# Performance work log

Hardware: AMD Instinct MI355X
Metric: run time of the kernel (lower is better)

## Reference

```python
import jax, jax.numpy as jnp
import numpy as np

N_NODES = 50000
N_EDGES = 1000000


def _gat_layer(x, edge_index, edge_prob, W, Wt, a_src, a_trg, a_tp, b, Wskip, concat):
    """One GATLayerImp3 forward (eval mode, dropout=identity).
    x: [N,Fin], edge_index: [2,E] (row0=src,row1=trg), edge_prob: [E,1].
    a_*: [1,H,F]. Returns [N,H*F] if concat else [N,F]."""
    N = x.shape[0]
    H, F = a_src.shape[1], a_src.shape[2]
    src, trg = edge_index[0], edge_index[1]

    proj = (x @ W).reshape(N, H, F)                      # [N,H,F]
    tp_proj = (edge_prob @ Wt).reshape(-1, H, F)         # [E,H,F]

    s_src = jnp.sum(proj * a_src, axis=-1)               # [N,H]
    s_trg = jnp.sum(proj * a_trg, axis=-1)               # [N,H]
    s_tp = jnp.sum(tp_proj * a_tp, axis=-1)              # [E,H]

    scores = jax.nn.leaky_relu(s_src[src] + s_trg[trg] + s_tp, 0.2)  # [E,H]
    exp_s = jnp.exp(scores - jnp.max(scores))            # global max, as in original
    denom = jax.ops.segment_sum(exp_s, trg, num_segments=N)[trg]     # [E,H]
    att = (exp_s / (denom + 1e-16))[:, :, None]          # [E,H,1]

    out = jax.ops.segment_sum(proj[src] * att, trg, num_segments=N)  # [N,H,F]

    if Wskip is None:  # dims match -> identity skip
        out = out + x[:, None, :]
    else:
        out = out + (x @ Wskip).reshape(N, H, F)

    out = out.reshape(N, H * F) if concat else out.mean(axis=1)
    return jax.nn.elu(out + b)


def setup_inputs() -> dict:
    key = jax.random.key(0)
    ks = jax.random.split(key, 16)
    s = 0.05
    return {
        "x": jax.random.normal(ks[0], (N_NODES, 128), jnp.float32),
        "edge_index": jax.random.randint(ks[1], (2, N_EDGES), 0, N_NODES, jnp.int32),
        "edge_prob": jax.random.uniform(ks[2], (N_EDGES, 1), jnp.float32),
        "W1": jax.random.normal(ks[3], (128, 128), jnp.float32) * s,
        "Wt1": jax.random.normal(ks[4], (1, 128), jnp.float32) * s,
        "a_src1": jax.random.normal(ks[5], (1, 8, 16), jnp.float32) * s,
        "a_trg1": jax.random.normal(ks[6], (1, 8, 16), jnp.float32) * s,
        "a_tp1": jax.random.normal(ks[7], (1, 8, 16), jnp.float32) * s,
        "b1": jnp.zeros((128,), jnp.float32),
        "Wskip1": jax.random.normal(ks[8], (128, 128), jnp.float32) * s,
        "W2": jax.random.normal(ks[9], (128, 128), jnp.float32) * s,
        "Wt2": jax.random.normal(ks[10], (1, 128), jnp.float32) * s,
        "a_src2": jax.random.normal(ks[11], (1, 1, 128), jnp.float32) * s,
        "a_trg2": jax.random.normal(ks[12], (1, 1, 128), jnp.float32) * s,
        "a_tp2": jax.random.normal(ks[13], (1, 1, 128), jnp.float32) * s,
        "b2": jnp.zeros((128,), jnp.float32),
    }


def reference(x, edge_index, edge_prob, W1, Wt1, a_src1, a_trg1, a_tp1, b1, Wskip1,
              W2, Wt2, a_src2, a_trg2, a_tp2, b2):
    h = _gat_layer(x, edge_index, edge_prob, W1, Wt1, a_src1, a_trg1, a_tp1, b1,
                   Wskip1, concat=True)                    # [N, 128]
    out = _gat_layer(h, edge_index, edge_prob, W2, Wt2, a_src2, a_trg2, a_tp2, b2,
                     None, concat=False)                   # [N, 128]
    return out
```

## Files before the change

### kernel.cpp

```cpp
#include <hip/hip_runtime.h>
#include <hip/hip_fp16.h>
#include <cstdint>
#include <cstddef>

__global__ __launch_bounds__(256) void gemm_dual(const float* __restrict__ A,
                                                 const float* __restrict__ B1,
                                                 const float* __restrict__ B2,
                                                 float* __restrict__ C1,
                                                 __half* __restrict__ Ch1,
                                                 float* __restrict__ C2, int M) {
  __shared__ float Ast[32][68];
  __shared__ float Bs1[32][132];
  __shared__ float Bs2[32][132];
  const int t = threadIdx.x;
  const int row0 = blockIdx.x * 64;
  const int ty = t >> 4, tx = t & 15;

  float acc1[4][8] = {};
  float acc2[4][8] = {};

  for (int kt = 0; kt < 4; ++kt) {
#pragma unroll
    for (int i = 0; i < 2; ++i) {
      int idx = t + i * 256;
      int r = idx >> 3;
      int kq = (idx & 7) * 4;
      float4 v = make_float4(0.f, 0.f, 0.f, 0.f);
      if (row0 + r < M)
        v = *reinterpret_cast<const float4*>(A + (size_t)(row0 + r) * 128 + kt * 32 + kq);
      Ast[kq + 0][r] = v.x;
      Ast[kq + 1][r] = v.y;
      Ast[kq + 2][r] = v.z;
      Ast[kq + 3][r] = v.w;
    }
#pragma unroll
    for (int i = 0; i < 4; ++i) {
      int idx = t + i * 256;
      int k = idx >> 5;
      int c4 = (idx & 31) * 4;
      *reinterpret_cast<float4*>(&Bs1[k][c4]) =
          *reinterpret_cast<const float4*>(B1 + (size_t)(kt * 32 + k) * 128 + c4);
      *reinterpret_cast<float4*>(&Bs2[k][c4]) =
          *reinterpret_cast<const float4*>(B2 + (size_t)(kt * 32 + k) * 128 + c4);
    }
    __syncthreads();

#pragma unroll
    for (int k = 0; k < 32; ++k) {
      float4 a4 = *reinterpret_cast<float4*>(&Ast[k][ty * 4]);
      float a[4] = {a4.x, a4.y, a4.z, a4.w};
      float4 p0 = *reinterpret_cast<float4*>(&Bs1[k][tx * 4]);
      float4 p1 = *reinterpret_cast<float4*>(&Bs1[k][64 + tx * 4]);
      float b1v[8] = {p0.x, p0.y, p0.z, p0.w, p1.x, p1.y, p1.z, p1.w};
      float4 q0 = *reinterpret_cast<float4*>(&Bs2[k][tx * 4]);
      float4 q1 = *reinterpret_cast<float4*>(&Bs2[k][64 + tx * 4]);
      float b2v[8] = {q0.x, q0.y, q0.z, q0.w, q1.x, q1.y, q1.z, q1.w};
#pragma unroll
      for (int i = 0; i < 4; ++i)
#pragma unroll
        for (int j = 0; j < 8; ++j) {
          acc1[i][j] += a[i] * b1v[j];
          acc2[i][j] += a[i] * b2v[j];
        }
    }
    __syncthreads();
  }

#pragma unroll
  for (int i = 0; i < 4; ++i) {
    int r = row0 + ty * 4 + i;
    if (r < M) {
      float4 lo = make_float4(acc1[i][0], acc1[i][1], acc1[i][2], acc1[i][3]);
      float4 hi = make_float4(acc1[i][4], acc1[i][5], acc1[i][6], acc1[i][7]);
      *reinterpret_cast<float4*>(C1 + (size_t)r * 128 + tx * 4) = lo;
      *reinterpret_cast<float4*>(C1 + (size_t)r * 128 + 64 + tx * 4) = hi;
      __half2* hp0 = reinterpret_cast<__half2*>(Ch1 + (size_t)r * 128 + tx * 4);
      __half2* hp1 = reinterpret_cast<__half2*>(Ch1 + (size_t)r * 128 + 64 + tx * 4);
      hp0[0] = __floats2half2_rn(lo.x, lo.y);
      hp0[1] = __floats2half2_rn(lo.z, lo.w);
      hp1[0] = __floats2half2_rn(hi.x, hi.y);
      hp1[1] = __floats2half2_rn(hi.z, hi.w);
      float4 lo2 = make_float4(acc2[i][0], acc2[i][1], acc2[i][2], acc2[i][3]);
      float4 hi2 = make_float4(acc2[i][4], acc2[i][5], acc2[i][6], acc2[i][7]);
      *reinterpret_cast<float4*>(C2 + (size_t)r * 128 + tx * 4) = lo2;
      *reinterpret_cast<float4*>(C2 + (size_t)r * 128 + 64 + tx * 4) = hi2;
    }
  }
}

__global__ __launch_bounds__(256) void gemm128_f32(const float* __restrict__ A,
                                                   const float* __restrict__ B,
                                                   float* __restrict__ C,
                                                   __half* __restrict__ Ch, int M) {
  __shared__ float Ast[32][68];
  __shared__ float Bs[32][132];
  const int t = threadIdx.x;
  const int row0 = blockIdx.x * 64;
  const int ty = t >> 4, tx = t & 15;

  float acc[4][8] = {};

  for (int kt = 0; kt < 4; ++kt) {
#pragma unroll
    for (int i = 0; i < 2; ++i) {
      int idx = t + i * 256;
      int r = idx >> 3;
      int kq = (idx & 7) * 4;
      float4 v = make_float4(0.f, 0.f, 0.f, 0.f);
      if (row0 + r < M)
        v = *reinterpret_cast<const float4*>(A + (size_t)(row0 + r) * 128 + kt * 32 + kq);
      Ast[kq + 0][r] = v.x;
      Ast[kq + 1][r] = v.y;
      Ast[kq + 2][r] = v.z;
      Ast[kq + 3][r] = v.w;
    }
#pragma unroll
    for (int i = 0; i < 4; ++i) {
      int idx = t + i * 256;
      int k = idx >> 5;
      int c4 = (idx & 31) * 4;
      *reinterpret_cast<float4*>(&Bs[k][c4]) =
          *reinterpret_cast<const float4*>(B + (size_t)(kt * 32 + k) * 128 + c4);
    }
    __syncthreads();

#pragma unroll
    for (int k = 0; k < 32; ++k) {
      float4 a4 = *reinterpret_cast<float4*>(&Ast[k][ty * 4]);
      float4 b0 = *reinterpret_cast<float4*>(&Bs[k][tx * 4]);
      float4 b1 = *reinterpret_cast<float4*>(&Bs[k][64 + tx * 4]);
      float a[4] = {a4.x, a4.y, a4.z, a4.w};
      float b[8] = {b0.x, b0.y, b0.z, b0.w, b1.x, b1.y, b1.z, b1.w};
#pragma unroll
      for (int i = 0; i < 4; ++i)
#pragma unroll
        for (int j = 0; j < 8; ++j) acc[i][j] += a[i] * b[j];
    }
    __syncthreads();
  }

#pragma unroll
  for (int i = 0; i < 4; ++i) {
    int r = row0 + ty * 4 + i;
    if (r < M) {
      float4 lo = make_float4(acc[i][0], acc[i][1], acc[i][2], acc[i][3]);
      float4 hi = make_float4(acc[i][4], acc[i][5], acc[i][6], acc[i][7]);
      *reinterpret_cast<float4*>(C + (size_t)r * 128 + tx * 4) = lo;
      *reinterpret_cast<float4*>(C + (size_t)r * 128 + 64 + tx * 4) = hi;
      if (Ch) {
        __half2* hp0 = reinterpret_cast<__half2*>(Ch + (size_t)r * 128 + tx * 4);
        __half2* hp1 = reinterpret_cast<__half2*>(Ch + (size_t)r * 128 + 64 + tx * 4);
        hp0[0] = __floats2half2_rn(lo.x, lo.y);
        hp0[1] = __floats2half2_rn(lo.z, lo.w);
        hp1[0] = __floats2half2_rn(hi.x, hi.y);
        hp1[1] = __floats2half2_rn(hi.z, hi.w);
      }
    }
  }
}

__global__ __launch_bounds__(256) void bucket_hist(const int* __restrict__ trg,
                                                   int* __restrict__ bhist, int E) {
  __shared__ int cnt[256];
  cnt[threadIdx.x] = 0;
  __syncthreads();
  const int base = blockIdx.x * 1024;
#pragma unroll
  for (int j = 0; j < 4; ++j) {
    int e = base + threadIdx.x + j * 256;
    if (e < E) atomicAdd(&cnt[trg[e] >> 8], 1);
  }
  __syncthreads();
  int c = cnt[threadIdx.x];
  if (c) atomicAdd(&bhist[threadIdx.x], c);
}

__global__ void scan196(const int* __restrict__ bhist, int* __restrict__ boffx,
                        int* __restrict__ bcur, int* __restrict__ row_off, int nb, int N) {
  __shared__ int s[256];
  int t = threadIdx.x;
  bcur[t] = 0;
  int v = (t < nb) ? bhist[t] : 0;
  s[t] = v;
  __syncthreads();
#pragma unroll
  for (int off = 1; off < 256; off <<= 1) {
    int x = s[t];
    int add = (t >= off) ? s[t - off] : 0;
    __syncthreads();
    s[t] = x + add;
    __syncthreads();
  }
  if (t < nb) boffx[t] = (t == 0) ? 0 : s[t - 1];
  if (t == 0) {
    boffx[nb] = s[255];
    row_off[N] = s[255];
  }
}

__global__ __launch_bounds__(256) void bucket_scatter(
    const int* __restrict__ src, const int* __restrict__ trg,
    const float* __restrict__ ep, const int* __restrict__ boffx,
    int* __restrict__ bcur, int2* __restrict__ staging, int E, int N) {
  __shared__ int cnt[256], boff[256], rowb[256];
  const int nb2 = (N + 255) >> 8;
  if (threadIdx.x < nb2) cnt[threadIdx.x] = 0;
  __syncthreads();
  const int base = blockIdx.x * 1024;
  int b_[4], r_[4], s_[4], p_[4];
#pragma unroll
  for (int j = 0; j < 4; ++j) {
    int e = base + threadIdx.x + j * 256;
    bool v = e < E;
    int tg = v ? trg[e] : 0;
    int sc = v ? src[e] : 0;
    p_[j] = v ? __float_as_int(ep[e]) : 0;
    b_[j] = tg >> 8;
    s_[j] = sc | ((tg & 255) << 16);
    r_[j] = v ? atomicAdd(&cnt[b_[j]], 1) : -1;
  }
  __syncthreads();
  if (threadIdx.x < nb2) {
    int c = cnt[threadIdx.x];
    boff[threadIdx.x] = c ? atomicAdd(&bcur[threadIdx.x], c) : 0;
    rowb[threadIdx.x] = boffx[threadIdx.x];
  }
  __syncthreads();
#pragma unroll
  for (int j = 0; j < 4; ++j) {
    if (r_[j] >= 0) {
      int b = b_[j];
      staging[rowb[b] + boff[b] + r_[j]] = make_int2(s_[j], p_[j]);
    }
  }
}

__global__ __launch_bounds__(256) void bucket_place(
    const int2* __restrict__ staging, const int* __restrict__ boffx,
    int* __restrict__ row_off, int2* __restrict__ edge2, int N) {
  __shared__ int cnt[256], loc[256], cur[256];
  const int t = threadIdx.x;
  const int n0 = blockIdx.x << 8;
  const int nn = min(256, N - n0);
  cnt[t] = 0;
  __syncthreads();
  const int lo = boffx[blockIdx.x];
  const int hi = boffx[blockIdx.x + 1];
  for (int i = lo + t; i < hi; i += 256) {
    atomicAdd(&cnt[(staging[i].x >> 16) & 255], 1);
  }
  __syncthreads();
  loc[t] = cnt[t];
  __syncthreads();
#pragma unroll
  for (int off = 1; off < 256; off <<= 1) {
    int x = loc[t];
    int add = (t >= off) ? loc[t - off] : 0;
    __syncthreads();
    loc[t] = x + add;
    __syncthreads();
  }
  int excl = loc[t] - cnt[t];
  if (t < nn) row_off[n0 + t] = lo + excl;
  cur[t] = lo + excl;
  __syncthreads();
  for (int i = lo + t; i < hi; i += 256) {
    int2 v = staging[i];
    int ln = (v.x >> 16) & 255;
    int pos = atomicAdd(&cur[ln], 1);
    edge2[pos] = make_int2(v.x & 0xFFFF, v.y);
  }
}

template <int H, int F>
__global__ void node_scores(const float* __restrict__ proj, const float* __restrict__ a_src,
                            const float* __restrict__ a_trg, float* __restrict__ ssrc,
                            float* __restrict__ strg, int N) {
  int idx = blockIdx.x * blockDim.x + threadIdx.x;
  if (idx >= N * H) return;
  int n = idx / H, h = idx % H;
  const float* p = proj + (size_t)n * (H * F) + h * F;
  const float* as = a_src + h * F;
  const float* at = a_trg + h * F;
  float d1 = 0.f, d2 = 0.f;
#pragma unroll
  for (int f = 0; f < F; f += 4) {
    float4 pv = *reinterpret_cast<const float4*>(p + f);
    float4 av = *reinterpret_cast<const float4*>(as + f);
    float4 tv = *reinterpret_cast<const float4*>(at + f);
    d1 += pv.x * av.x + pv.y * av.y + pv.z * av.z + pv.w * av.w;
    d2 += pv.x * tv.x + pv.y * tv.y + pv.z * tv.z + pv.w * tv.w;
  }
  ssrc[idx] = d1;
  strg[idx] = d2;
}

template <int H, int F>
__global__ void aggregate(const int2* __restrict__ edge2, const int* __restrict__ row_off,
                          const float* __restrict__ ssrc, const float* __restrict__ strg,
                          const float* __restrict__ Wt, const float* __restrict__ a_tp,
                          const __half* __restrict__ projh, const float* __restrict__ skip,
                          const float* __restrict__ bias, float* __restrict__ out, int N) {
  static_assert(H * F == 128, "offset shift assumes H*F==128");
  int wid = (blockIdx.x * blockDim.x + threadIdx.x) >> 6;
  if (wid >= N) return;
  const int lane = threadIdx.x & 63;
  const int half = lane >> 5;
  const int fl = (lane & 31) * 4;
  const int h = fl / F;

  float4 wt4 = *reinterpret_cast<const float4*>(Wt + fl);
  float4 at4 = *reinterpret_cast<const float4*>(a_tp + fl);
  float ch = wt4.x * at4.x + wt4.y * at4.y + wt4.z * at4.z + wt4.w * at4.w;
#pragma unroll
  for (int off = 1; off < (F / 4); off <<= 1) ch += __shfl_xor(ch, off);

  const float mt = strg[wid * H + h];
  const int beg = row_off[wid];
  const int end = row_off[wid + 1];

  float ax = 0.f, ay = 0.f, az = 0.f, aw = 0.f;
  float denom = 0.f;

  for (int i = beg; i < end; i += 8) {
    int   s[4];
    float pe[4], vd[4];
    float2 raw[4];
#pragma unroll
    for (int q = 0; q < 4; ++q) {
      int ii = i + q * 2 + half;
      bool v = ii < end;
      int2 e2 = v ? edge2[ii] : make_int2(0, 0);
      s[q] = e2.x;
      pe[q] = __int_as_float(e2.y);
      vd[q] = v ? 1.f : 0.f;
    }
#pragma unroll
    for (int q = 0; q < 4; ++q)
      raw[q] = *reinterpret_cast<const float2*>(projh + (s[q] << 7) + fl);
#pragma unroll
    for (int q = 0; q < 4; ++q) {
      float sc = ssrc[s[q] * H + h] + mt + pe[q] * ch;
      sc = sc > 0.f ? sc : 0.2f * sc;
      float ee = __expf(sc) * vd[q];
      __half2 h01 = *reinterpret_cast<__half2*>(&raw[q].x);
      __half2 h23 = *reinterpret_cast<__half2*>(&raw[q].y);
      float2 f01 = __half22float2(h01);
      float2 f23 = __half22float2(h23);
      denom += ee;
      ax += f01.x * ee;
      ay += f01.y * ee;
      az += f23.x * ee;
      aw += f23.y * ee;
    }
  }

  denom += __shfl_xor(denom, 32);
  ax += __shfl_xor(ax, 32);
  ay += __shfl_xor(ay, 32);
  az += __shfl_xor(az, 32);
  aw += __shfl_xor(aw, 32);

  if (half == 0) {
    float inv = 1.0f / (denom + 1e-16f);
    int base = (wid << 7) + fl;
    float4 sk = *reinterpret_cast<const float4*>(skip + base);
    float4 bi = *reinterpret_cast<const float4*>(bias + fl);
    float o0 = ax * inv + sk.x + bi.x;
    float o1 = ay * inv + sk.y + bi.y;
    float o2 = az * inv + sk.z + bi.z;
    float o3 = aw * inv + sk.w + bi.w;
    o0 = o0 > 0.f ? o0 : __expf(o0) - 1.f;
    o1 = o1 > 0.f ? o1 : __expf(o1) - 1.f;
    o2 = o2 > 0.f ? o2 : __expf(o2) - 1.f;
    o3 = o3 > 0.f ? o3 : __expf(o3) - 1.f;
    float4 ov = make_float4(o0, o1, o2, o3);
    *reinterpret_cast<float4*>(out + base) = ov;
  }
}

extern "C" void kernel_launch(void* const* d_in, const int* in_sizes, int n_in,
                              void* d_out, int out_size, void* d_ws, size_t ws_size,
                              hipStream_t stream) {
  const float* x      = (const float*)d_in[0];
  const int*   ei     = (const int*)  d_in[1];
  const float* ep     = (const float*)d_in[2];
  const float* W1     = (const float*)d_in[3];
  const float* Wt1    = (const float*)d_in[4];
  const float* a_src1 = (const float*)d_in[5];
  const float* a_trg1 = (const float*)d_in[6];
  const float* a_tp1  = (const float*)d_in[7];
  const float* b1     = (const float*)d_in[8];
  const float* Wskip1 = (const float*)d_in[9];
  const float* W2     = (const float*)d_in[10];
  const float* Wt2    = (const float*)d_in[11];
  const float* a_src2 = (const float*)d_in[12];
  const float* a_trg2 = (const float*)d_in[13];
  const float* a_tp2  = (const float*)d_in[14];
  const float* b2     = (const float*)d_in[15];

  const int N = in_sizes[0] / 128;
  const int E = in_sizes[1] / 2;
  const int* srcA = ei;
  const int* trgA = ei + E;

  char* ws = (char*)d_ws;
  size_t off = 0;
  auto alloc = [&](size_t bytes) {
    void* p = ws + off;
    off += (bytes + 255) & ~(size_t)255;
    return p;
  };
  int*    bhist   = (int*)   alloc((size_t)256 * 4);
  int*    bcur    = (int*)   alloc((size_t)256 * 4);
  int*    boffx   = (int*)   alloc((size_t)257 * 4);
  int*    row_off = (int*)   alloc((size_t)(N + 1) * 4);
  int2*   staging = (int2*)  alloc((size_t)E * 8);
  int2*   edge2   = (int2*)  alloc((size_t)E * 8);
  float*  proj    = (float*) alloc((size_t)N * 128 * 4);
  __half* projh   = (__half*)alloc((size_t)N * 128 * 2);
  float*  skip1   = (float*) alloc((size_t)N * 128 * 4);
  float*  hbuf    = (float*) alloc((size_t)N * 128 * 4);
  float*  ssrc    = (float*) alloc((size_t)N * 8 * 4);
  float*  strg    = (float*) alloc((size_t)N * 8 * 4);
  (void)ws_size; (void)n_in; (void)out_size;

  hipMemsetAsync(bhist, 0, 256 * 4, stream);

  const int eb4 = (E + 1023) / 1024;
  const int gb = (N + 63) / 64;
  const int nb = (N + 255) / 256;

  bucket_hist<<<eb4, 256, 0, stream>>>(trgA, bhist, E);
  scan196<<<1, 256, 0, stream>>>(bhist, boffx, bcur, row_off, nb, N);
  bucket_scatter<<<eb4, 256, 0, stream>>>(srcA, trgA, ep, boffx, bcur, staging, E, N);
  bucket_place<<<nb, 256, 0, stream>>>(staging, boffx, row_off, edge2, N);

  gemm_dual<<<gb, 256, 0, stream>>>(x, W1, Wskip1, proj, projh, skip1, N);
  node_scores<8, 16><<<(N * 8 + 255) / 256, 256, 0, stream>>>(proj, a_src1, a_trg1, ssrc, strg, N);
  aggregate<8, 16><<<(N + 3) / 4, 256, 0, stream>>>(edge2, row_off, ssrc, strg, Wt1, a_tp1,
                                                    projh, skip1, b1, hbuf, N);

  gemm128_f32<<<gb, 256, 0, stream>>>(hbuf, W2, proj, projh, N);
  node_scores<1, 128><<<(N + 255) / 256, 256, 0, stream>>>(proj, a_src2, a_trg2, ssrc, strg, N);
  aggregate<1, 128><<<(N + 3) / 4, 256, 0, stream>>>(edge2, row_off, ssrc, strg, Wt2, a_tp2,
                                                     projh, hbuf, b2, (float*)d_out, N);
}
```

Before: 405.4 us.

## Replace FP32 SIMT GEMMs with FP16 MFMA and keep intermediates in half

The scalar FP32 shared-memory GEMMs are replaced with MFMA 16x16x32 f16 kernels that read pre-packed half weights and a half copy of x. The skip, hidden and projection buffers become half precision, so node_scores and aggregate read fp16 data and layer 1 writes its output in fp16. The aim is to cut GEMM compute time and the memory traffic of the intermediates. The cost is extra pack and convert launches plus lower precision in the skip path and hidden activations, which could affect accuracy.

```diff
diff --git a/kernel.cpp b/kernel.cpp
--- a/kernel.cpp
+++ b/kernel.cpp
@@ -3,157 +3,95 @@
 #include <cstdint>
 #include <cstddef>
 
-__global__ __launch_bounds__(256) void gemm_dual(const float* __restrict__ A,
-                                                 const float* __restrict__ B1,
-                                                 const float* __restrict__ B2,
-                                                 float* __restrict__ C1,
-                                                 __half* __restrict__ Ch1,
-                                                 float* __restrict__ C2, int M) {
-  __shared__ float Ast[32][68];
-  __shared__ float Bs1[32][132];
-  __shared__ float Bs2[32][132];
-  const int t = threadIdx.x;
-  const int row0 = blockIdx.x * 64;
-  const int ty = t >> 4, tx = t & 15;
-
-  float acc1[4][8] = {};
-  float acc2[4][8] = {};
-
+typedef _Float16 half8 __attribute__((ext_vector_type(8)));
+typedef float f32x4 __attribute__((ext_vector_type(4)));
+
+__global__ void pack_b(const float* __restrict__ B, __half* __restrict__ Bp) {
+  int slot = blockIdx.x * 256 + threadIdx.x;
+  int lane = slot & 63;
+  int nt = (slot >> 6) & 7;
+  int kt = slot >> 9;
+  int r0 = kt * 32 + (lane >> 4) * 8;
+  int col = nt * 16 + (lane & 15);
+  __half tmp[8];
+#pragma unroll
+  for (int j = 0; j < 8; ++j) tmp[j] = __float2half(B[(r0 + j) * 128 + col]);
+  *reinterpret_cast<float4*>(Bp + (size_t)slot * 8) = *reinterpret_cast<float4*>(tmp);
+}
+
+__global__ void f32_to_f16(const float* __restrict__ in, __half* __restrict__ out, int n8) {
+  int i = blockIdx.x * 256 + threadIdx.x;
+  if (i >= n8) return;
+  float4 a = *reinterpret_cast<const float4*>(in + (size_t)i * 8);
+  float4 b = *reinterpret_cast<const float4*>(in + (size_t)i * 8 + 4);
+  __half2 h[4] = {__floats2half2_rn(a.x, a.y), __floats2half2_rn(a.z, a.w),
+                  __floats2half2_rn(b.x, b.y), __floats2half2_rn(b.z, b.w)};
+  *reinterpret_cast<float4*>(out + (size_t)i * 8) = *reinterpret_cast<float4*>(h);
+}
+
+__global__ __launch_bounds__(256) void gemm_mfma(const __half* __restrict__ Ah,
+                                                 const half8* __restrict__ Bp,
+                                                 __half* __restrict__ C, int M) {
+  const int w = threadIdx.x >> 6, lane = threadIdx.x & 63;
+  const int row0 = blockIdx.x * 64 + w * 16;
+  const int arow = row0 + (lane & 15);
+  const int kb = (lane >> 4) * 8;
+  const bool av = arow < M;
+  f32x4 acc[8] = {};
   for (int kt = 0; kt < 4; ++kt) {
-#pragma unroll
-    for (int i = 0; i < 2; ++i) {
-      int idx = t + i * 256;
-      int r = idx >> 3;
-      int kq = (idx & 7) * 4;
-      float4 v = make_float4(0.f, 0.f, 0.f, 0.f);
-      if (row0 + r < M)
-        v = *reinterpret_cast<const float4*>(A + (size_t)(row0 + r) * 128 + kt * 32 + kq);
-      Ast[kq + 0][r] = v.x;
-      Ast[kq + 1][r] = v.y;
-      Ast[kq + 2][r] = v.z;
-      Ast[kq + 3][r] = v.w;
-    }
-#pragma unroll
-    for (int i = 0; i < 4; ++i) {
-      int idx = t + i * 256;
-      int k = idx >> 5;
-      int c4 = (idx & 31) * 4;
-      *reinterpret_cast<float4*>(&Bs1[k][c4]) =
-          *reinterpret_cast<const float4*>(B1 + (size_t)(kt * 32 + k) * 128 + c4);
-      *reinterpret_cast<float4*>(&Bs2[k][c4]) =
-          *reinterpret_cast<const float4*>(B2 + (size_t)(kt * 32 + k) * 128 + c4);
-    }
-    __syncthreads();
-
-#pragma unroll
-    for (int k = 0; k < 32; ++k) {
-      float4 a4 = *reinterpret_cast<float4*>(&Ast[k][ty * 4]);
-      float a[4] = {a4.x, a4.y, a4.z, a4.w};
-      float4 p0 = *reinterpret_cast<float4*>(&Bs1[k][tx * 4]);
-      float4 p1 = *reinterpret_cast<float4*>(&Bs1[k][64 + tx * 4]);
-      float b1v[8] = {p0.x, p0.y, p0.z, p0.w, p1.x, p1.y, p1.z, p1.w};
-      float4 q0 = *reinterpret_cast<float4*>(&Bs2[k][tx * 4]);
-      float4 q1 = *reinterpret_cast<float4*>(&Bs2[k][64 + tx * 4]);
-      float b2v[8] = {q0.x, q0.y, q0.z, q0.w, q1.x, q1.y, q1.z, q1.w};
-#pragma unroll
-      for (int i = 0; i < 4; ++i)
-#pragma unroll
-        for (int j = 0; j < 8; ++j) {
-          acc1[i][j] += a[i] * b1v[j];
-          acc2[i][j] += a[i] * b2v[j];
-        }
-    }
-    __syncthreads();
-  }
-
-#pragma unroll
-  for (int i = 0; i < 4; ++i) {
-    int r = row0 + ty * 4 + i;
-    if (r < M) {
-      float4 lo = make_float4(acc1[i][0], acc1[i][1], acc1[i][2], acc1[i][3]);
-      float4 hi = make_float4(acc1[i][4], acc1[i][5], acc1[i][6], acc1[i][7]);
-      *reinterpret_cast<float4*>(C1 + (size_t)r * 128 + tx * 4) = lo;
-      *reinterpret_cast<float4*>(C1 + (size_t)r * 128 + 64 + tx * 4) = hi;
-      __half2* hp0 = reinterpret_cast<__half2*>(Ch1 + (size_t)r * 128 + tx * 4);
-      __half2* hp1 = reinterpret_cast<__half2*>(Ch1 + (size_t)r * 128 + 64 + tx * 4);
-      hp0[0] = __floats2half2_rn(lo.x, lo.y);
-      hp0[1] = __floats2half2_rn(lo.z, lo.w);
-      hp1[0] = __floats2half2_rn(hi.x, hi.y);
-      hp1[1] = __floats2half2_rn(hi.z, hi.w);
-      float4 lo2 = make_float4(acc2[i][0], acc2[i][1], acc2[i][2], acc2[i][3]);
-      float4 hi2 = make_float4(acc2[i][4], acc2[i][5], acc2[i][6], acc2[i][7]);
-      *reinterpret_cast<float4*>(C2 + (size_t)r * 128 + tx * 4) = lo2;
-      *reinterpret_cast<float4*>(C2 + (size_t)r * 128 + 64 + tx * 4) = hi2;
-    }
-  }
-}
-
-__global__ __launch_bounds__(256) void gemm128_f32(const float* __restrict__ A,
-                                                   const float* __restrict__ B,
-                                                   float* __restrict__ C,
-                                                   __half* __restrict__ Ch, int M) {
-  __shared__ float Ast[32][68];
-  __shared__ float Bs[32][132];
-  const int t = threadIdx.x;
-  const int row0 = blockIdx.x * 64;
-  const int ty = t >> 4, tx = t & 15;
-
-  float acc[4][8] = {};
-
+    half8 af = {};
+    if (av) af = *reinterpret_cast<const half8*>(Ah + (size_t)arow * 128 + kt * 32 + kb);
+    const half8* bb = Bp + (kt * 8) * 64 + lane;
+#pragma unroll
+    for (int nt = 0; nt < 8; ++nt)
+      acc[nt] = __builtin_amdgcn_mfma_f32_16x16x32_f16(af, bb[nt * 64], acc[nt], 0, 0, 0);
+  }
+  const int orow = row0 + (lane >> 4) * 4;
+  const int col = lane & 15;
+#pragma unroll
+  for (int r = 0; r < 4; ++r) {
+    int rr = orow + r;
+    if (rr < M) {
+#pragma unroll
+      for (int nt = 0; nt < 8; ++nt)
+        C[(size_t)rr * 128 + nt * 16 + col] = __float2half(acc[nt][r]);
+    }
+  }
+}
+
+__global__ __launch_bounds__(256) void gemm_mfma_dual(const __half* __restrict__ Ah,
+                                                      const half8* __restrict__ Bp1,
+                                                      const half8* __restrict__ Bp2,
+                                                      __half* __restrict__ C1,
+                                                      __half* __restrict__ C2, int M) {
+  const int w = threadIdx.x >> 6, lane = threadIdx.x & 63;
+  const int row0 = blockIdx.x * 64 + w * 16;
+  const int arow = row0 + (lane & 15);
+  const int kb = (lane >> 4) * 8;
+  const bool av = arow < M;
+  f32x4 acc1[8] = {};
+  f32x4 acc2[8] = {};
   for (int kt = 0; kt < 4; ++kt) {
-#pragma unroll
-    for (int i = 0; i < 2; ++i) {
-      int idx = t + i * 256;
-      int r = idx >> 3;
-      int kq = (idx & 7) * 4;
-      float4 v = make_float4(0.f, 0.f, 0.f, 0.f);
-      if (row0 + r < M)
-        v = *reinterpret_cast<const float4*>(A + (size_t)(row0 + r) * 128 + kt * 32 + kq);
-      Ast[kq + 0][r] = v.x;
-      Ast[kq + 1][r] = v.y;
-      Ast[kq + 2][r] = v.z;
-      Ast[kq + 3][r] = v.w;
-    }
-#pragma unroll
-    for (int i = 0; i < 4; ++i) {
-      int idx = t + i * 256;
-      int k = idx >> 5;
-      int c4 = (idx & 31) * 4;
-      *reinterpret_cast<float4*>(&Bs[k][c4]) =
-          *reinterpret_cast<const float4*>(B + (size_t)(kt * 32 + k) * 128 + c4);
-    }
-    __syncthreads();
-
-#pragma unroll
-    for (int k = 0; k < 32; ++k) {
-      float4 a4 = *reinterpret_cast<float4*>(&Ast[k][ty * 4]);
-      float4 b0 = *reinterpret_cast<float4*>(&Bs[k][tx * 4]);
-      float4 b1 = *reinterpret_cast<float4*>(&Bs[k][64 + tx * 4]);
-      float a[4] = {a4.x, a4.y, a4.z, a4.w};
-      float b[8] = {b0.x, b0.y, b0.z, b0.w, b1.x, b1.y, b1.z, b1.w};
-#pragma unroll
-      for (int i = 0; i < 4; ++i)
-#pragma unroll
-        for (int j = 0; j < 8; ++j) acc[i][j] += a[i] * b[j];
-    }
-    __syncthreads();
-  }
-
-#pragma unroll
-  for (int i = 0; i < 4; ++i) {
-    int r = row0 + ty * 4 + i;
-    if (r < M) {
-      float4 lo = make_float4(acc[i][0], acc[i][1], acc[i][2], acc[i][3]);
-      float4 hi = make_float4(acc[i][4], acc[i][5], acc[i][6], acc[i][7]);
-      *reinterpret_cast<float4*>(C + (size_t)r * 128 + tx * 4) = lo;
-      *reinterpret_cast<float4*>(C + (size_t)r * 128 + 64 + tx * 4) = hi;
-      if (Ch) {
-        __half2* hp0 = reinterpret_cast<__half2*>(Ch + (size_t)r * 128 + tx * 4);
-        __half2* hp1 = reinterpret_cast<__half2*>(Ch + (size_t)r * 128 + 64 + tx * 4);
-        hp0[0] = __floats2half2_rn(lo.x, lo.y);
-        hp0[1] = __floats2half2_rn(lo.z, lo.w);
-        hp1[0] = __floats2half2_rn(hi.x, hi.y);
-        hp1[1] = __floats2half2_rn(hi.z, hi.w);
+    half8 af = {};
+    if (av) af = *reinterpret_cast<const half8*>(Ah + (size_t)arow * 128 + kt * 32 + kb);
+    const half8* b1 = Bp1 + (kt * 8) * 64 + lane;
+    const half8* b2 = Bp2 + (kt * 8) * 64 + lane;
+#pragma unroll
+    for (int nt = 0; nt < 8; ++nt) {
+      acc1[nt] = __builtin_amdgcn_mfma_f32_16x16x32_f16(af, b1[nt * 64], acc1[nt], 0, 0, 0);
+      acc2[nt] = __builtin_amdgcn_mfma_f32_16x16x32_f16(af, b2[nt * 64], acc2[nt], 0, 0, 0);
+    }
+  }
+  const int orow = row0 + (lane >> 4) * 4;
+  const int col = lane & 15;
+#pragma unroll
+  for (int r = 0; r < 4; ++r) {
+    int rr = orow + r;
+    if (rr < M) {
+#pragma unroll
+      for (int nt = 0; nt < 8; ++nt) {
+        C1[(size_t)rr * 128 + nt * 16 + col] = __float2half(acc1[nt][r]);
+        C2[(size_t)rr * 128 + nt * 16 + col] = __float2half(acc2[nt][r]);
       }
     }
   }
@@ -273,34 +211,43 @@
 }
 
 template <int H, int F>
-__global__ void node_scores(const float* __restrict__ proj, const float* __restrict__ a_src,
-                            const float* __restrict__ a_trg, float* __restrict__ ssrc,
-                            float* __restrict__ strg, int N) {
+__global__ void node_scores_h(const __half* __restrict__ projh, const float* __restrict__ a_src,
+                              const float* __restrict__ a_trg, float* __restrict__ ssrc,
+                              float* __restrict__ strg, int N) {
   int idx = blockIdx.x * blockDim.x + threadIdx.x;
   if (idx >= N * H) return;
   int n = idx / H, h = idx % H;
-  const float* p = proj + (size_t)n * (H * F) + h * F;
+  const __half* p = projh + (size_t)n * (H * F) + h * F;
   const float* as = a_src + h * F;
   const float* at = a_trg + h * F;
   float d1 = 0.f, d2 = 0.f;
 #pragma unroll
-  for (int f = 0; f < F; f += 4) {
-    float4 pv = *reinterpret_cast<const float4*>(p + f);
-    float4 av = *reinterpret_cast<const float4*>(as + f);
-    float4 tv = *reinterpret_cast<const float4*>(at + f);
-    d1 += pv.x * av.x + pv.y * av.y + pv.z * av.z + pv.w * av.w;
-    d2 += pv.x * tv.x + pv.y * tv.y + pv.z * tv.z + pv.w * tv.w;
+  for (int f = 0; f < F; f += 8) {
+    float4 raw = *reinterpret_cast<const float4*>(p + f);
+    const __half2* hp = reinterpret_cast<const __half2*>(&raw);
+    float2 p01 = __half22float2(hp[0]);
+    float2 p23 = __half22float2(hp[1]);
+    float2 p45 = __half22float2(hp[2]);
+    float2 p67 = __half22float2(hp[3]);
+    float4 a0 = *reinterpret_cast<const float4*>(as + f);
+    float4 a1 = *reinterpret_cast<const float4*>(as + f + 4);
+    float4 t0 = *reinterpret_cast<const float4*>(at + f);
+    float4 t1 = *reinterpret_cast<const float4*>(at + f + 4);
+    d1 += p01.x * a0.x + p01.y * a0.y + p23.x * a0.z + p23.y * a0.w +
+          p45.x * a1.x + p45.y * a1.y + p67.x * a1.z + p67.y * a1.w;
+    d2 += p01.x * t0.x + p01.y * t0.y + p23.x * t0.z + p23.y * t0.w +
+          p45.x * t1.x + p45.y * t1.y + p67.x * t1.z + p67.y * t1.w;
   }
   ssrc[idx] = d1;
   strg[idx] = d2;
 }
 
-template <int H, int F>
+template <int H, int F, bool OUT_F16>
 __global__ void aggregate(const int2* __restrict__ edge2, const int* __restrict__ row_off,
                           const float* __restrict__ ssrc, const float* __restrict__ strg,
                           const float* __restrict__ Wt, const float* __restrict__ a_tp,
-                          const __half* __restrict__ projh, const float* __restrict__ skip,
-                          const float* __restrict__ bias, float* __restrict__ out, int N) {
+                          const __half* __restrict__ projh, const __half* __restrict__ skiph,
+                          const float* __restrict__ bias, void* __restrict__ outv, int N) {
   static_assert(H * F == 128, "offset shift assumes H*F==128");
   int wid = (blockIdx.x * blockDim.x + threadIdx.x) >> 6;
   if (wid >= N) return;
@@ -364,18 +311,30 @@
   if (half == 0) {
     float inv = 1.0f / (denom + 1e-16f);
     int base = (wid << 7) + fl;
-    float4 sk = *reinterpret_cast<const float4*>(skip + base);
+    float2 skraw = *reinterpret_cast<const float2*>(skiph + base);
+    const __half2* sp = reinterpret_cast<const __half2*>(&skraw);
+    float2 s01 = __half22float2(sp[0]);
+    float2 s23 = __half22float2(sp[1]);
     float4 bi = *reinterpret_cast<const float4*>(bias + fl);
-    float o0 = ax * inv + sk.x + bi.x;
-    float o1 = ay * inv + sk.y + bi.y;
-    float o2 = az * inv + sk.z + bi.z;
-    float o3 = aw * inv + sk.w + bi.w;
+    float o0 = ax * inv + s01.x + bi.x;
+    float o1 = ay * inv + s01.y + bi.y;
+    float o2 = az * inv + s23.x + bi.z;
+    float o3 = aw * inv + s23.y + bi.w;
     o0 = o0 > 0.f ? o0 : __expf(o0) - 1.f;
     o1 = o1 > 0.f ? o1 : __expf(o1) - 1.f;
     o2 = o2 > 0.f ? o2 : __expf(o2) - 1.f;
     o3 = o3 > 0.f ? o3 : __expf(o3) - 1.f;
-    float4 ov = make_float4(o0, o1, o2, o3);
-    *reinterpret_cast<float4*>(out + base) = ov;
+    if (OUT_F16) {
+      __half2 w01 = __floats2half2_rn(o0, o1);
+      __half2 w23 = __floats2half2_rn(o2, o3);
+      float2 wv;
+      reinterpret_cast<__half2*>(&wv)[0] = w01;
+      reinterpret_cast<__half2*>(&wv)[1] = w23;
+      *reinterpret_cast<float2*>(reinterpret_cast<__half*>(outv) + base) = wv;
+    } else {
+      *reinterpret_cast<float4*>(reinterpret_cast<float*>(outv) + base) =
+          make_float4(o0, o1, o2, o3);
+    }
   }
 }
 
@@ -417,10 +376,13 @@
   int*    row_off = (int*)   alloc((size_t)(N + 1) * 4);
   int2*   staging = (int2*)  alloc((size_t)E * 8);
   int2*   edge2   = (int2*)  alloc((size_t)E * 8);
-  float*  proj    = (float*) alloc((size_t)N * 128 * 4);
+  __half* xh      = (__half*)alloc((size_t)N * 128 * 2);
   __half* projh   = (__half*)alloc((size_t)N * 128 * 2);
-  float*  skip1   = (float*) alloc((size_t)N * 128 * 4);
-  float*  hbuf    = (float*) alloc((size_t)N * 128 * 4);
+  __half* skiph   = (__half*)alloc((size_t)N * 128 * 2);
+  __half* hbufh   = (__half*)alloc((size_t)N * 128 * 2);
+  __half* Bp1     = (__half*)alloc((size_t)2048 * 8 * 2);
+  __half* BpS     = (__half*)alloc((size_t)2048 * 8 * 2);
+  __half* Bp2     = (__half*)alloc((size_t)2048 * 8 * 2);
   float*  ssrc    = (float*) alloc((size_t)N * 8 * 4);
   float*  strg    = (float*) alloc((size_t)N * 8 * 4);
   (void)ws_size; (void)n_in; (void)out_size;
@@ -430,19 +392,28 @@
   const int eb4 = (E + 1023) / 1024;
   const int gb = (N + 63) / 64;
   const int nb = (N + 255) / 256;
+
+  f32_to_f16<<<(N * 16 + 255) / 256, 256, 0, stream>>>(x, xh, N * 16);
+  pack_b<<<8, 256, 0, stream>>>(W1, Bp1);
+  pack_b<<<8, 256, 0, stream>>>(Wskip1, BpS);
+  pack_b<<<8, 256, 0, stream>>>(W2, Bp2);
 
   bucket_hist<<<eb4, 256, 0, stream>>>(trgA, bhist, E);
   scan196<<<1, 256, 0, stream>>>(bhist, boffx, bcur, row_off, nb, N);
   bucket_scatter<<<eb4, 256, 0, stream>>>(srcA, trgA, ep, boffx, bcur, staging, E, N);
   bucket_place<<<nb, 256, 0, stream>>>(staging, boffx, row_off, edge2, N);
 
-  gemm_dual<<<gb, 256, 0, stream>>>(x, W1, Wskip1, proj, projh, skip1, N);
-  node_scores<8, 16><<<(N * 8 + 255) / 256, 256, 0, stream>>>(proj, a_src1, a_trg1, ssrc, strg, N);
-  aggregate<8, 16><<<(N + 3) / 4, 256, 0, stream>>>(edge2, row_off, ssrc, strg, Wt1, a_tp1,
-                                                    projh, skip1, b1, hbuf, N);
-
-  gemm128_f32<<<gb, 256, 0, stream>>>(hbuf, W2, proj, projh, N);
-  node_scores<1, 128><<<(N + 255) / 256, 256, 0, stream>>>(proj, a_src2, a_trg2, ssrc, strg, N);
-  aggregate<1, 128><<<(N + 3) / 4, 256, 0, stream>>>(edge2, row_off, ssrc, strg, Wt2, a_tp2,
-                                                     projh, hbuf, b2, (float*)d_out, N);
-}
+  gemm_mfma_dual<<<gb, 256, 0, stream>>>(xh, (const half8*)Bp1, (const half8*)BpS,
+                                         projh, skiph, N);
+  node_scores_h<8, 16><<<(N * 8 + 255) / 256, 256, 0, stream>>>(projh, a_src1, a_trg1,
+                                                                ssrc, strg, N);
+  aggregate<8, 16, true><<<(N + 3) / 4, 256, 0, stream>>>(edge2, row_off, ssrc, strg, Wt1,
+                                                          a_tp1, projh, skiph, b1, hbufh, N);
+
+  gemm_mfma<<<gb, 256, 0, stream>>>(hbufh, (const half8*)Bp2, projh, N);
+  node_scores_h<1, 128><<<(N + 255) / 256, 256, 0, stream>>>(projh, a_src2, a_trg2,
+                                                             ssrc, strg, N);
+  aggregate<1, 128, false><<<(N + 3) / 4, 256, 0, stream>>>(edge2, row_off, ssrc, strg, Wt2,
+                                                            a_tp2, projh, hbufh, b2,
+                                                            (float*)d_out, N);
+}
```

Result: faster. 344.8 us (-15.0%).
